# Performance work log

Hardware: AMD Instinct MI355X
Metric: run time of the kernel (lower is better)

Reference implementation:

```python
import jax, jax.numpy as jnp
import numpy as np

B = 1024       # repertoires (batch)
TCR = 100      # instances (TCRs) per repertoire
FEAT = 15      # feature_num (conv in_channels)
AA = 24        # aa_num (sequence length)
KS = [2, 3, 4, 5, 6, 7]
FN = [3, 3, 3, 2, 2, 1]
NINP = 14      # sum(FN)
EPS = 1e-5     # BatchNorm eps


def sparsemax(z):
    # z: (B, K); sparsemax along axis 1 (Martins & Astudillo 2016)
    K = z.shape[1]
    zs = -jnp.sort(-z, axis=1)               # descending sort
    cs = jnp.cumsum(zs, axis=1)
    k = jnp.arange(1, K + 1, dtype=z.dtype)
    support = 1.0 + k * zs > cs              # (B, K) bool
    ksel = jnp.sum(support, axis=1, keepdims=True).astype(jnp.int32)  # support size
    tau = (jnp.take_along_axis(cs, ksel - 1, axis=1) - 1.0) / ksel.astype(z.dtype)
    return jnp.maximum(z - tau, 0.0)


def setup_inputs() -> dict:
    key = jax.random.key(0)
    ks = jax.random.split(key, 12)
    inp = {"x": jax.random.normal(ks[0], (B, TCR, FEAT, AA), dtype=jnp.float32)}
    for i, (h, f) in enumerate(zip(KS, FN)):
        inp[f"cw{i}"] = jax.random.normal(ks[1 + i], (f, FEAT, h), dtype=jnp.float32) * 0.1
        inp[f"cb{i}"] = jnp.zeros((f,), dtype=jnp.float32)
    inp["fc1_w"] = jax.random.normal(ks[7], (NINP, NINP), dtype=jnp.float32) * 0.2
    inp["fc1_b"] = jnp.zeros((NINP,), dtype=jnp.float32)
    inp["waout_w"] = jax.random.normal(ks[8], (1, NINP), dtype=jnp.float32) * 0.2
    inp["decf_w"] = jax.random.normal(ks[9], (NINP, NINP), dtype=jnp.float32) * 0.2
    inp["decf_b"] = jnp.zeros((NINP,), dtype=jnp.float32)
    inp["bn_g"] = jnp.ones((NINP,), dtype=jnp.float32)
    inp["bn_b"] = jnp.zeros((NINP,), dtype=jnp.float32)
    inp["decs_w"] = jax.random.normal(ks[10], (2, NINP), dtype=jnp.float32) * 0.2
    inp["decs_b"] = jnp.zeros((2,), dtype=jnp.float32)
    return inp


def reference(x, cw0, cb0, cw1, cb1, cw2, cb2, cw3, cb3, cw4, cb4, cw5, cb5,
              fc1_w, fc1_b, waout_w, decf_w, decf_b, bn_g, bn_b, decs_w, decs_b):
    xf = x.reshape(-1, FEAT, AA)  # (B*TCR, 15, 24)
    feats = []
    for w, b in ((cw0, cb0), (cw1, cb1), (cw2, cb2), (cw3, cb3), (cw4, cb4), (cw5, cb5)):
        y = jax.lax.conv_general_dilated(xf, w, (1,), 'VALID',
                                         dimension_numbers=('NCH', 'OIH', 'NCH'))
        y = jax.nn.relu(y + b[None, :, None])
        feats.append(jnp.max(y, axis=-1))  # AdaptiveMaxPool1d(1): global max over length
    out = jnp.concatenate(feats, axis=1).reshape(-1, TCR, NINP)  # (B, TCR, 14)
    # fclayer1 + dropout(eval=identity) + relu; applied per-instance so the
    # torch (TCR, B, .) transpose is equivalent to working in (B, TCR, .)
    h = jax.nn.relu(out @ fc1_w.T + fc1_b)                       # (B, TCR, 14)
    attw = sparsemax(h @ waout_w[0])                             # (B, TCR)
    pooled = jnp.einsum('bt,btd->bd', attw, h)                   # bmm(attw[:,None,:], h)
    z = pooled @ decf_w.T + decf_b                               # decoder_f
    mu = jnp.mean(z, axis=0)                                     # BatchNorm1d (batch stats)
    var = jnp.var(z, axis=0)
    z = jax.nn.relu((z - mu) / jnp.sqrt(var + EPS) * bn_g + bn_b)
    logits = z @ decs_w.T + decs_b                               # decoder_s -> (B, 2)
    return logits, attw
```

## Files before the change

kernel.cpp:

```cpp
#include <hip/hip_runtime.h>

typedef unsigned int  u32;
typedef unsigned short u16;

__device__ __forceinline__ float bf2f(u16 u){
    return __uint_as_float(((u32)u) << 16);
}
__device__ __forceinline__ float lo16(u32 v){ return __uint_as_float(v << 16); }
__device__ __forceinline__ float hi16(u32 v){ return __uint_as_float(v & 0xffff0000u); }
__device__ __forceinline__ u16 f2bf(float f){
    u32 x = __float_as_uint(f);
    x += 0x7fffu + ((x >> 16) & 1u);
    return (u16)(x >> 16);
}
__device__ __forceinline__ float ldany(const void* p, int i, bool bf){
    return bf ? bf2f(((const u16*)p)[i]) : ((const float*)p)[i];
}

#define B_      1024
#define TCR_    100
#define NINST   (B_*TCR_)

#define OFF_WCH    0
#define OFF_CB     840
#define OFF_FC1W   854
#define OFF_FC1B   1050
#define OFF_WA     1064
#define OFF_DECFW  1078
#define OFF_DECFB  1274
#define OFF_BNG    1288
#define OFF_BNB    1302
#define OFF_DECSW  1316
#define OFF_DECSB  1344

__global__ __launch_bounds__(256) void k_pack(
    const void* cw0, const void* cb0, const void* cw1, const void* cb1,
    const void* cw2, const void* cb2, const void* cw3, const void* cb3,
    const void* cw4, const void* cb4, const void* cw5, const void* cb5,
    const void* fc1_w, const void* fc1_b, const void* waout,
    const void* decf_w, const void* decf_b,
    const void* bn_g, const void* bn_b,
    const void* decs_w, const void* decs_b,
    float* __restrict__ wsP)
{
    const int tid = threadIdx.x;
    const bool bf = (((const u16*)bn_g)[0] == 0x3F80u);

    for (int widx = tid; widx < 840; widx += 256){
        float val; int dst;
        if (widx < 90)      { int e = widx;       int c=e/6,  rr=e-c*6,  ff=rr/2, j=rr-ff*2; val=ldany(cw0,(ff*15+c)*2+j,bf); dst=c*56+ 0+ff*2+j; }
        else if (widx < 225){ int e = widx - 90;  int c=e/9,  rr=e-c*9,  ff=rr/3, j=rr-ff*3; val=ldany(cw1,(ff*15+c)*3+j,bf); dst=c*56+ 6+ff*3+j; }
        else if (widx < 405){ int e = widx - 225; int c=e/12, rr=e-c*12, ff=rr/4, j=rr-ff*4; val=ldany(cw2,(ff*15+c)*4+j,bf); dst=c*56+15+ff*4+j; }
        else if (widx < 555){ int e = widx - 405; int c=e/10, rr=e-c*10, ff=rr/5, j=rr-ff*5; val=ldany(cw3,(ff*15+c)*5+j,bf); dst=c*56+27+ff*5+j; }
        else if (widx < 735){ int e = widx - 555; int c=e/12, rr=e-c*12, ff=rr/6, j=rr-ff*6; val=ldany(cw4,(ff*15+c)*6+j,bf); dst=c*56+37+ff*6+j; }
        else                { int e = widx - 735; int c=e/7,  j=e-c*7;                        val=ldany(cw5,c*7+j,bf);        dst=c*56+49+j; }
        wsP[OFF_WCH + dst] = val;
    }
    for (int i = tid; i < 14; i += 256){
        float bv;
        if (i < 3)       bv = ldany(cb0, i, bf);
        else if (i < 6)  bv = ldany(cb1, i - 3, bf);
        else if (i < 9)  bv = ldany(cb2, i - 6, bf);
        else if (i < 11) bv = ldany(cb3, i - 9, bf);
        else if (i < 13) bv = ldany(cb4, i - 11, bf);
        else             bv = ldany(cb5, 0, bf);
        wsP[OFF_CB    + i] = bv;
        wsP[OFF_FC1B  + i] = ldany(fc1_b,  i, bf);
        wsP[OFF_WA    + i] = ldany(waout,  i, bf);
        wsP[OFF_DECFB + i] = ldany(decf_b, i, bf);
        wsP[OFF_BNG   + i] = ldany(bn_g,   i, bf);
        wsP[OFF_BNB   + i] = ldany(bn_b,   i, bf);
    }
    for (int i = tid; i < 196; i += 256){
        wsP[OFF_FC1W  + i] = ldany(fc1_w,  i, bf);
        wsP[OFF_DECFW + i] = ldany(decf_w, i, bf);
    }
    for (int i = tid; i < 28; i += 256) wsP[OFF_DECSW + i] = ldany(decs_w, i, bf);
    for (int i = tid; i < 2;  i += 256) wsP[OFF_DECSB + i] = ldany(decs_b, i, bf);
}

template<int H, int F, int GOFF>
__device__ __forceinline__ void acc_ch(float (&acc)[F][17 - H], const float* xr,
                                       const float* __restrict__ wch){
    float wv[F * H];
    #pragma unroll
    for (int k = 0; k < F * H; ++k) wv[k] = wch[GOFF + k];
    #pragma unroll
    for (int ff = 0; ff < F; ++ff)
        #pragma unroll
        for (int i = 0; i < 17 - H; ++i)
            #pragma unroll
            for (int j = 0; j < H; ++j)
                acc[ff][i] = fmaf(wv[ff * H + j], xr[i + j], acc[ff][i]);
}

template<int H, int F, int OF>
__device__ __forceinline__ void pair_max(float (&acc)[F][17 - H],
                                         const float* __restrict__ wsP, float* feats){
    #pragma unroll
    for (int ff = 0; ff < F; ++ff){
        float m = acc[ff][0];
        #pragma unroll
        for (int i = 1; i < 17 - H; ++i) m = fmaxf(m, acc[ff][i]);
        m = fmaxf(m, __shfl_xor(m, 1));
        feats[OF + ff] = fmaxf(m + wsP[OFF_CB + OF + ff], 0.0f);
    }
}

template<bool BF>
__device__ __forceinline__ void unpack16(const uint4* buf, float* xr){
    if (BF){
        #pragma unroll
        for (int i = 0; i < 2; ++i){
            u32 w0 = buf[i].x, w1 = buf[i].y, w2 = buf[i].z, w3 = buf[i].w;
            xr[i*8+0] = lo16(w0); xr[i*8+1] = hi16(w0);
            xr[i*8+2] = lo16(w1); xr[i*8+3] = hi16(w1);
            xr[i*8+4] = lo16(w2); xr[i*8+5] = hi16(w2);
            xr[i*8+6] = lo16(w3); xr[i*8+7] = hi16(w3);
        }
    } else {
        #pragma unroll
        for (int i = 0; i < 4; ++i){
            xr[i*4+0] = __uint_as_float(buf[i].x);
            xr[i*4+1] = __uint_as_float(buf[i].y);
            xr[i*4+2] = __uint_as_float(buf[i].z);
            xr[i*4+3] = __uint_as_float(buf[i].w);
        }
    }
}

template<bool BF>
__device__ __forceinline__ void conv_body(const void* __restrict__ x,
                                          const float* __restrict__ wsP,
                                          float* __restrict__ hbufT,
                                          float* __restrict__ sbuf){
    constexpr int NB = BF ? 2 : 4;
    constexpr int CS = BF ? 48 : 96;
    const int tid   = threadIdx.x;
    const int tpart = tid & 1;
    const int inst  = blockIdx.x * 128 + (tid >> 1);
    const char* xb  = (const char*)x + (size_t)inst * (BF ? 720 : 1440)
                                     + tpart * (BF ? 16 : 32);

    float a2[3][15], a3[3][14], a4[3][13], a5[2][12], a6[2][11], a7[1][10];
    #pragma unroll
    for (int f = 0; f < 3; ++f){
        #pragma unroll
        for (int i = 0; i < 15; ++i) a2[f][i] = 0.0f;
        #pragma unroll
        for (int i = 0; i < 14; ++i) a3[f][i] = 0.0f;
        #pragma unroll
        for (int i = 0; i < 13; ++i) a4[f][i] = 0.0f;
    }
    #pragma unroll
    for (int f = 0; f < 2; ++f){
        #pragma unroll
        for (int i = 0; i < 12; ++i) a5[f][i] = 0.0f;
        #pragma unroll
        for (int i = 0; i < 11; ++i) a6[f][i] = 0.0f;
    }
    #pragma unroll
    for (int i = 0; i < 10; ++i) a7[0][i] = 0.0f;

    uint4 cur[NB];
    {
        const uint4* p = (const uint4*)xb;
        #pragma unroll
        for (int i = 0; i < NB; ++i) cur[i] = p[i];
    }
    #pragma unroll 1
    for (int c = 0; c < 15; ++c){
        uint4 nxt[NB];
        int cn = (c < 14) ? (c + 1) : 14;
        const uint4* pn = (const uint4*)(xb + cn * CS);
        #pragma unroll
        for (int i = 0; i < NB; ++i) nxt[i] = pn[i];

        float xr[16];
        unpack16<BF>(cur, xr);
        const float* wch = wsP + OFF_WCH + c * 56;
        acc_ch<2,3, 0>(a2, xr, wch);
        acc_ch<3,3, 6>(a3, xr, wch);
        acc_ch<4,3,15>(a4, xr, wch);
        acc_ch<5,2,27>(a5, xr, wch);
        acc_ch<6,2,37>(a6, xr, wch);
        acc_ch<7,1,49>(a7, xr, wch);

        #pragma unroll
        for (int i = 0; i < NB; ++i) cur[i] = nxt[i];
    }

    float feats[14];
    pair_max<2,3, 0>(a2, wsP, feats);
    pair_max<3,3, 3>(a3, wsP, feats);
    pair_max<4,3, 6>(a4, wsP, feats);
    pair_max<5,2, 9>(a5, wsP, feats);
    pair_max<6,2,11>(a6, wsP, feats);
    pair_max<7,1,13>(a7, wsP, feats);

    float hv[14];
    #pragma unroll
    for (int i = 0; i < 14; ++i){
        float a = wsP[OFF_FC1B + i];
        #pragma unroll
        for (int j = 0; j < 14; ++j) a = fmaf(feats[j], wsP[OFF_FC1W + i * 14 + j], a);
        hv[i] = fmaxf(a, 0.0f);
    }
    float sc = 0.0f;
    #pragma unroll
    for (int i = 0; i < 14; ++i) sc = fmaf(hv[i], wsP[OFF_WA + i], sc);

    if (tpart == 0){
        #pragma unroll
        for (int d = 0; d < 14; ++d) hbufT[d * NINST + inst] = hv[d];
        sbuf[inst] = sc;
    }
}

__global__ __launch_bounds__(256) void k_conv(
    const void* __restrict__ x, const float* __restrict__ wsP,
    const void* __restrict__ dt,
    float* __restrict__ hbufT, float* __restrict__ sbuf)
{
    const bool bf = (((const u16*)dt)[0] == 0x3F80u);
    if (bf) conv_body<true >(x, wsP, hbufT, sbuf);
    else    conv_body<false>(x, wsP, hbufT, sbuf);
}

__global__ __launch_bounds__(64) void k_sparse(
    const float* __restrict__ hbufT, const float* __restrict__ sbuf,
    const float* __restrict__ wsP, const void* __restrict__ dt,
    float* __restrict__ zbuf, void* __restrict__ d_out)
{
    const int b    = blockIdx.x;
    const int lane = threadIdx.x;
    const bool bf  = (((const u16*)dt)[0] == 0x3F80u);
    const bool has2 = lane < (TCR_ - 64);

    float z0 = sbuf[b * TCR_ + lane];
    float z1 = has2 ? sbuf[b * TCR_ + 64 + lane] : -1e30f;

    float m = fmaxf(z0, z1);
    #pragma unroll
    for (int o = 32; o; o >>= 1) m = fmaxf(m, __shfl_xor(m, o));

    float lo = m - 1.0f, hi = m;
    for (int it = 0; it < 16; ++it){
        float mid = 0.5f * (lo + hi);
        float s = fmaxf(z0 - mid, 0.0f) + fmaxf(z1 - mid, 0.0f);
        #pragma unroll
        for (int o = 32; o; o >>= 1) s += __shfl_xor(s, o);
        if (s >= 1.0f) lo = mid; else hi = mid;
    }
    float tm = 0.5f * (lo + hi);
    float i0 = (z0 > tm) ? 1.0f : 0.0f;
    float i1 = (z1 > tm) ? 1.0f : 0.0f;
    float sz = i0 * z0 + i1 * z1;
    float kc = i0 + i1;
    #pragma unroll
    for (int o = 32; o; o >>= 1){ sz += __shfl_xor(sz, o); kc += __shfl_xor(kc, o); }
    float tau = (sz - 1.0f) / kc;

    float a0 = fmaxf(z0 - tau, 0.0f);
    float a1 = fmaxf(z1 - tau, 0.0f);

    if (bf){
        u16* aw = (u16*)d_out + 2048;
        aw[b * TCR_ + lane] = f2bf(a0);
        if (has2) aw[b * TCR_ + 64 + lane] = f2bf(a1);
    } else {
        float* aw = (float*)d_out + 2048;
        aw[b * TCR_ + lane] = a0;
        if (has2) aw[b * TCR_ + 64 + lane] = a1;
    }

    float ap[14];
    #pragma unroll
    for (int d = 0; d < 14; ++d){
        float v = a0 * hbufT[d * NINST + b * TCR_ + lane];
        if (has2) v += a1 * hbufT[d * NINST + b * TCR_ + 64 + lane];
        #pragma unroll
        for (int o = 32; o; o >>= 1) v += __shfl_xor(v, o);
        ap[d] = v;
    }
    if (lane < 14){
        float zv = wsP[OFF_DECFB + lane];
        #pragma unroll
        for (int j = 0; j < 14; ++j) zv = fmaf(ap[j], wsP[OFF_DECFW + lane * 14 + j], zv);
        zbuf[b * 14 + lane] = zv;
    }
}

__global__ __launch_bounds__(256) void k_bn(
    const float* __restrict__ zbuf, const float* __restrict__ wsP,
    const void* __restrict__ dt, void* __restrict__ d_out)
{
    __shared__ float part[4][28];
    __shared__ float red[28];
    const int tid  = threadIdx.x;
    const int lane = tid & 63;
    const int w    = tid >> 6;
    const bool bf  = (((const u16*)dt)[0] == 0x3F80u);

    float z[4][14];
    #pragma unroll
    for (int r = 0; r < 4; ++r)
        #pragma unroll
        for (int d = 0; d < 14; ++d) z[r][d] = zbuf[(tid + 256 * r) * 14 + d];

    #pragma unroll
    for (int d = 0; d < 14; ++d){
        float s = 0.0f, q = 0.0f;
        #pragma unroll
        for (int r = 0; r < 4; ++r){ s += z[r][d]; q += z[r][d] * z[r][d]; }
        #pragma unroll
        for (int o = 32; o; o >>= 1){ s += __shfl_xor(s, o); q += __shfl_xor(q, o); }
        if (lane == 0){ part[w][d] = s; part[w][14 + d] = q; }
    }
    __syncthreads();
    if (tid < 28) red[tid] = part[0][tid] + part[1][tid] + part[2][tid] + part[3][tid];
    __syncthreads();

    float mu[14], rs[14];
    #pragma unroll
    for (int d = 0; d < 14; ++d){
        mu[d] = red[d] * (1.0f / 1024.0f);
        float var = red[14 + d] * (1.0f / 1024.0f) - mu[d] * mu[d];
        rs[d] = rsqrtf(var + 1e-5f);
    }
    #pragma unroll
    for (int r = 0; r < 4; ++r){
        float zn[14];
        #pragma unroll
        for (int d = 0; d < 14; ++d)
            zn[d] = fmaxf((z[r][d] - mu[d]) * rs[d] * wsP[OFF_BNG + d] + wsP[OFF_BNB + d], 0.0f);
        #pragma unroll
        for (int c = 0; c < 2; ++c){
            float a = wsP[OFF_DECSB + c];
            #pragma unroll
            for (int d = 0; d < 14; ++d) a = fmaf(zn[d], wsP[OFF_DECSW + c * 14 + d], a);
            if (bf) ((u16*)d_out)[(tid + 256 * r) * 2 + c] = f2bf(a);
            else    ((float*)d_out)[(tid + 256 * r) * 2 + c] = a;
        }
    }
}

extern "C" void kernel_launch(void* const* d_in, const int* in_sizes, int n_in,
                              void* d_out, int out_size, void* d_ws, size_t ws_size,
                              hipStream_t stream)
{
    (void)in_sizes; (void)n_in; (void)out_size; (void)ws_size;
    const void* x     = d_in[0];
    const void* bn_g  = d_in[18];

    float* wsP   = (float*)d_ws;
    float* hbufT = wsP + 2048;
    float* sbuf  = hbufT + (size_t)14 * NINST;
    float* zbuf  = sbuf + NINST;

    k_pack<<<1, 256, 0, stream>>>(
        d_in[1], d_in[2], d_in[3], d_in[4], d_in[5], d_in[6],
        d_in[7], d_in[8], d_in[9], d_in[10], d_in[11], d_in[12],
        d_in[13], d_in[14], d_in[15], d_in[16], d_in[17],
        d_in[18], d_in[19], d_in[20], d_in[21], wsP);
    k_conv<<<NINST / 128, 256, 0, stream>>>(x, wsP, bn_g, hbufT, sbuf);
    k_sparse<<<B_, 64, 0, stream>>>(hbufT, sbuf, wsP, bn_g, zbuf, d_out);
    k_bn<<<1, 256, 0, stream>>>(zbuf, wsP, bn_g, d_out);
}
```

Baseline: 295.8 us.

## Split each conv instance across four threads with DPP quad max reduction

```diff
diff --git a/kernel.cpp b/kernel.cpp
--- a/kernel.cpp
+++ b/kernel.cpp
@@ -32,6 +32,17 @@
 #define OFF_BNB    1302
 #define OFF_DECSW  1316
 #define OFF_DECSB  1344
+
+template<int CTRL, int RM, int BM, bool BC>
+__device__ __forceinline__ float dpp_mv(float old_, float x){
+    return __int_as_float(__builtin_amdgcn_update_dpp(
+        __float_as_int(old_), __float_as_int(x), CTRL, RM, BM, BC));
+}
+__device__ __forceinline__ float qmax_quad(float m){
+    m = fmaxf(m, dpp_mv<0xB1,0xf,0xf,false>(m, m));
+    m = fmaxf(m, dpp_mv<0x4E,0xf,0xf,false>(m, m));
+    return m;
+}
 
 __global__ __launch_bounds__(256) void k_pack(
     const void* cw0, const void* cb0, const void* cw1, const void* cb1,
@@ -80,7 +91,7 @@
 }
 
 template<int H, int F, int GOFF>
-__device__ __forceinline__ void acc_ch(float (&acc)[F][17 - H], const float* xr,
+__device__ __forceinline__ void acc_ch(float (&acc)[F][13 - H], const float* xr,
                                        const float* __restrict__ wch){
     float wv[F * H];
     #pragma unroll
@@ -88,44 +99,48 @@
     #pragma unroll
     for (int ff = 0; ff < F; ++ff)
         #pragma unroll
-        for (int i = 0; i < 17 - H; ++i)
+        for (int i = 0; i < 13 - H; ++i)
             #pragma unroll
             for (int j = 0; j < H; ++j)
                 acc[ff][i] = fmaf(wv[ff * H + j], xr[i + j], acc[ff][i]);
 }
 
 template<int H, int F, int OF>
-__device__ __forceinline__ void pair_max(float (&acc)[F][17 - H],
+__device__ __forceinline__ void quad_max(float (&acc)[F][13 - H],
                                          const float* __restrict__ wsP, float* feats){
     #pragma unroll
     for (int ff = 0; ff < F; ++ff){
         float m = acc[ff][0];
         #pragma unroll
-        for (int i = 1; i < 17 - H; ++i) m = fmaxf(m, acc[ff][i]);
-        m = fmaxf(m, __shfl_xor(m, 1));
+        for (int i = 1; i < 13 - H; ++i) m = fmaxf(m, acc[ff][i]);
+        m = qmax_quad(m);
         feats[OF + ff] = fmaxf(m + wsP[OFF_CB + OF + ff], 0.0f);
     }
 }
 
 template<bool BF>
-__device__ __forceinline__ void unpack16(const uint4* buf, float* xr){
+__device__ __forceinline__ void ld_win(const char* p, u32* w){
     if (BF){
-        #pragma unroll
-        for (int i = 0; i < 2; ++i){
-            u32 w0 = buf[i].x, w1 = buf[i].y, w2 = buf[i].z, w3 = buf[i].w;
-            xr[i*8+0] = lo16(w0); xr[i*8+1] = hi16(w0);
-            xr[i*8+2] = lo16(w1); xr[i*8+3] = hi16(w1);
-            xr[i*8+4] = lo16(w2); xr[i*8+5] = hi16(w2);
-            xr[i*8+6] = lo16(w3); xr[i*8+7] = hi16(w3);
-        }
+        const uint2* q = (const uint2*)p;
+        uint2 a = q[0], b = q[1], c = q[2];
+        w[0]=a.x; w[1]=a.y; w[2]=b.x; w[3]=b.y; w[4]=c.x; w[5]=c.y;
     } else {
-        #pragma unroll
-        for (int i = 0; i < 4; ++i){
-            xr[i*4+0] = __uint_as_float(buf[i].x);
-            xr[i*4+1] = __uint_as_float(buf[i].y);
-            xr[i*4+2] = __uint_as_float(buf[i].z);
-            xr[i*4+3] = __uint_as_float(buf[i].w);
-        }
+        const uint4* q = (const uint4*)p;
+        uint4 a = q[0], b = q[1], c = q[2];
+        w[0]=a.x; w[1]=a.y; w[2]=a.z;  w[3]=a.w;
+        w[4]=b.x; w[5]=b.y; w[6]=b.z;  w[7]=b.w;
+        w[8]=c.x; w[9]=c.y; w[10]=c.z; w[11]=c.w;
+    }
+}
+
+template<bool BF>
+__device__ __forceinline__ void unpack12(const u32* w, float* xr){
+    if (BF){
+        #pragma unroll
+        for (int i = 0; i < 6; ++i){ xr[2*i] = lo16(w[i]); xr[2*i+1] = hi16(w[i]); }
+    } else {
+        #pragma unroll
+        for (int i = 0; i < 12; ++i) xr[i] = __uint_as_float(w[i]);
     }
 }
 
@@ -134,50 +149,44 @@
                                           const float* __restrict__ wsP,
                                           float* __restrict__ hbufT,
                                           float* __restrict__ sbuf){
-    constexpr int NB = BF ? 2 : 4;
+    constexpr int NW = BF ? 6 : 12;
     constexpr int CS = BF ? 48 : 96;
-    const int tid   = threadIdx.x;
-    const int tpart = tid & 1;
-    const int inst  = blockIdx.x * 128 + (tid >> 1);
-    const char* xb  = (const char*)x + (size_t)inst * (BF ? 720 : 1440)
-                                     + tpart * (BF ? 16 : 32);
-
-    float a2[3][15], a3[3][14], a4[3][13], a5[2][12], a6[2][11], a7[1][10];
+    const int tid  = threadIdx.x;
+    const int q    = tid & 3;
+    const int inst = blockIdx.x * 64 + (tid >> 2);
+    const char* xb = (const char*)x + (size_t)inst * (BF ? 720 : 1440)
+                                    + q * (BF ? 8 : 16);
+
+    float a2[3][11], a3[3][10], a4[3][9], a5[2][8], a6[2][7], a7[1][6];
     #pragma unroll
     for (int f = 0; f < 3; ++f){
         #pragma unroll
-        for (int i = 0; i < 15; ++i) a2[f][i] = 0.0f;
-        #pragma unroll
-        for (int i = 0; i < 14; ++i) a3[f][i] = 0.0f;
-        #pragma unroll
-        for (int i = 0; i < 13; ++i) a4[f][i] = 0.0f;
+        for (int i = 0; i < 11; ++i) a2[f][i] = 0.0f;
+        #pragma unroll
+        for (int i = 0; i < 10; ++i) a3[f][i] = 0.0f;
+        #pragma unroll
+        for (int i = 0; i < 9;  ++i) a4[f][i] = 0.0f;
     }
     #pragma unroll
     for (int f = 0; f < 2; ++f){
         #pragma unroll
-        for (int i = 0; i < 12; ++i) a5[f][i] = 0.0f;
-        #pragma unroll
-        for (int i = 0; i < 11; ++i) a6[f][i] = 0.0f;
-    }
-    #pragma unroll
-    for (int i = 0; i < 10; ++i) a7[0][i] = 0.0f;
-
-    uint4 cur[NB];
-    {
-        const uint4* p = (const uint4*)xb;
-        #pragma unroll
-        for (int i = 0; i < NB; ++i) cur[i] = p[i];
-    }
+        for (int i = 0; i < 8; ++i) a5[f][i] = 0.0f;
+        #pragma unroll
+        for (int i = 0; i < 7; ++i) a6[f][i] = 0.0f;
+    }
+    #pragma unroll
+    for (int i = 0; i < 6; ++i) a7[0][i] = 0.0f;
+
+    u32 cur[NW];
+    ld_win<BF>(xb, cur);
     #pragma unroll 1
     for (int c = 0; c < 15; ++c){
-        uint4 nxt[NB];
+        u32 nxt[NW];
         int cn = (c < 14) ? (c + 1) : 14;
-        const uint4* pn = (const uint4*)(xb + cn * CS);
-        #pragma unroll
-        for (int i = 0; i < NB; ++i) nxt[i] = pn[i];
-
-        float xr[16];
-        unpack16<BF>(cur, xr);
+        ld_win<BF>(xb + cn * CS, nxt);
+
+        float xr[12];
+        unpack12<BF>(cur, xr);
         const float* wch = wsP + OFF_WCH + c * 56;
         acc_ch<2,3, 0>(a2, xr, wch);
         acc_ch<3,3, 6>(a3, xr, wch);
@@ -187,16 +196,16 @@
         acc_ch<7,1,49>(a7, xr, wch);
 
         #pragma unroll
-        for (int i = 0; i < NB; ++i) cur[i] = nxt[i];
+        for (int i = 0; i < NW; ++i) cur[i] = nxt[i];
     }
 
     float feats[14];
-    pair_max<2,3, 0>(a2, wsP, feats);
-    pair_max<3,3, 3>(a3, wsP, feats);
-    pair_max<4,3, 6>(a4, wsP, feats);
-    pair_max<5,2, 9>(a5, wsP, feats);
-    pair_max<6,2,11>(a6, wsP, feats);
-    pair_max<7,1,13>(a7, wsP, feats);
+    quad_max<2,3, 0>(a2, wsP, feats);
+    quad_max<3,3, 3>(a3, wsP, feats);
+    quad_max<4,3, 6>(a4, wsP, feats);
+    quad_max<5,2, 9>(a5, wsP, feats);
+    quad_max<6,2,11>(a6, wsP, feats);
+    quad_max<7,1,13>(a7, wsP, feats);
 
     float hv[14];
     #pragma unroll
@@ -210,14 +219,14 @@
     #pragma unroll
     for (int i = 0; i < 14; ++i) sc = fmaf(hv[i], wsP[OFF_WA + i], sc);
 
-    if (tpart == 0){
+    if (q == 0){
         #pragma unroll
         for (int d = 0; d < 14; ++d) hbufT[d * NINST + inst] = hv[d];
         sbuf[inst] = sc;
     }
 }
 
-__global__ __launch_bounds__(256) void k_conv(
+__global__ __launch_bounds__(256, 3) void k_conv(
     const void* __restrict__ x, const float* __restrict__ wsP,
     const void* __restrict__ dt,
     float* __restrict__ hbufT, float* __restrict__ sbuf)
@@ -363,7 +372,7 @@
         d_in[7], d_in[8], d_in[9], d_in[10], d_in[11], d_in[12],
         d_in[13], d_in[14], d_in[15], d_in[16], d_in[17],
         d_in[18], d_in[19], d_in[20], d_in[21], wsP);
-    k_conv<<<NINST / 128, 256, 0, stream>>>(x, wsP, bn_g, hbufT, sbuf);
+    k_conv<<<NINST / 64, 256, 0, stream>>>(x, wsP, bn_g, hbufT, sbuf);
     k_sparse<<<B_, 64, 0, stream>>>(hbufT, sbuf, wsP, bn_g, zbuf, d_out);
     k_bn<<<1, 256, 0, stream>>>(zbuf, wsP, bn_g, d_out);
 }
```

Measured after the change: 307.8 us. 4.1% more time.
